# Kernel optimization log

Measured on AMD Instinct MI355X. Metric: run time of the kernel, lower is better.

The kernel has to match this reference:

```python
import jax, jax.numpy as jnp
import numpy as np

NUM_IT = 5            # init_kwargs num_it
N_NODES = 200_000
N_EDGES = 6_400_000   # avg degree 32
N_INIT_COLORS = 16

# odd 32-bit mixing constants (Knuth / xxhash primes); uint32 mults wrap mod 2^32
M1 = np.uint32(2654435761)
M2 = np.uint32(2246822519)
M3 = np.uint32(3266489917)
M4 = np.uint32(668265263)


def setup_inputs() -> dict:
    key = jax.random.key(0)
    k1, k2 = jax.random.split(key)
    x = jax.random.randint(k1, (N_NODES,), 0, N_INIT_COLORS, dtype=jnp.int32)
    edge_index = jax.random.randint(k2, (2, N_EDGES), 0, N_NODES, dtype=jnp.int32)
    return {"x": x, "edge_index": edge_index}


def _wl_iteration(colors, row, col, num_nodes):
    """One WLConv step: new color = id of (own color, sorted multiset of neighbor colors).

    The torch WLConv sorts each node's neighbor colors, hashes the tuple, and
    assigns compact ids via a dict. Here we do the same math vectorized:
    lexsort edges by (row, neighbor color), compute a position-weighted 2x32-bit
    hash of the sorted per-node sequence via segment_sum, mix in the node's own
    color, then relabel distinct keys to compact ids 0..k-1 with jnp.unique.
    """
    E = row.shape[0]
    c = colors[col]                                   # neighbor colors per edge [E]
    order = jnp.lexsort((c, row))                     # sort by node, then by color
    r_s = row[order]                                  # [E] sorted rows
    c_s = c[order].astype(jnp.uint32)                 # [E] sorted neighbor colors

    ones = jnp.ones((E,), dtype=jnp.int32)
    deg = jax.ops.segment_sum(ones, row, num_segments=num_nodes)      # [N]
    start = jnp.cumsum(deg) - deg                                     # segment offsets [N]
    pos = (jnp.arange(E, dtype=jnp.int32) - start[r_s]).astype(jnp.uint32)  # rank within node

    # two independent position-weighted hash lanes over each sorted neighbor list
    lane1 = jax.ops.segment_sum((c_s + 1) * (pos * M1 + M2), r_s, num_segments=num_nodes)
    lane2 = jax.ops.segment_sum((c_s + 1) * (pos * M3 + M4), r_s, num_segments=num_nodes)

    own = colors.astype(jnp.uint32) + 1
    key2 = jnp.stack([lane1 * M2 + own * M1, lane2 * M4 + own * M3], axis=1)  # [N,2]

    # dict-style relabeling: distinct keys -> compact ids (at most N distinct)
    _, inv = jnp.unique(key2, axis=0, size=num_nodes, return_inverse=True,
                        fill_value=jnp.uint32(0))
    return inv.reshape(-1).astype(colors.dtype)


def reference(x, edge_index):
    row, col = edge_index[0], edge_index[1]
    colors = x.astype(jnp.int32)
    for _ in range(NUM_IT):  # fixed small layer loop, not a data-dim loop
        colors = _wl_iteration(colors, row, col, N_NODES)
    return colors
```

## Files before the change

kernel.cpp:

```cpp
#include <hip/hip_runtime.h>
#include <stdint.h>

typedef unsigned int u32;
typedef unsigned long long u64;

#define M1 2654435761u
#define M2 2246822519u
#define M3 3266489917u
#define M4 668265263u
#define NUM_IT 5
#define PCHUNK 16384
#define HCH 65536
#define TILE 4096
#define PBCH 4096
#define CCAP 16384
#define SB 64
#define CHB 33
#define NKB 1024
#define KCH 4096
#define SCH 8192


__global__ void k_init(const int* __restrict__ x, int* __restrict__ colors,
                       u32* __restrict__ bcnt5, u32* __restrict__ bhist,
                       u32* __restrict__ cnt3, int n, int nbuck) {
    int i = blockIdx.x * blockDim.x + threadIdx.x;
    if (i < n) colors[i] = x[i];
    if (i < NUM_IT * NKB) bcnt5[i] = 0u;
    if (i >= 8192 && i < 8192 + nbuck) bhist[i - 8192] = 0u;
    if (i >= 16384 && i < 16384 + 48) cnt3[i - 16384] = 0u;
}

__global__ void k_chist(const int* __restrict__ row, u32* __restrict__ bhist,
                        u32* __restrict__ thist, int e, int nbuck) {
    __shared__ u32 fineh[1024];
    __shared__ u32 shist[16 * SB];
    int t = threadIdx.x;
    fineh[t] = 0u;
    shist[t] = 0u;
    __syncthreads();
    int c0 = blockIdx.x * HCH;
    int ce = c0 + HCH; if (ce > e) ce = e;
    int k = 0;
    for (int i = c0 + t; i < ce; i += 1024, ++k) {
        u32 r = (u32)row[i];
        atomicAdd(&fineh[r >> 8], 1u);
        atomicAdd(&shist[((k >> 2) << 6) | (r >> 12)], 1u);
    }
    __syncthreads();
    if (t < nbuck) {
        u32 v = fineh[t];
        if (v) atomicAdd(&bhist[t], v);
    }
    {
        int m = t >> 6;
        if (c0 + m * TILE < e)
            thist[(size_t)(blockIdx.x * 16 + m) * SB + (t & 63)] = shist[t];
    }
}

__global__ void k_cscan(const u32* __restrict__ bhist, u32* __restrict__ boffE,
                        u32* __restrict__ bcur, u32* __restrict__ boffS,
                        int nbuck, int nbS) {
    __shared__ u32 sh[256];
    u32 run = 0u;
    for (int base = 0; base < nbuck; base += 256) {
        int id = base + threadIdx.x;
        u32 x = (id < nbuck) ? bhist[id] : 0u;
        sh[threadIdx.x] = x;
        __syncthreads();
        for (int o = 1; o < 256; o <<= 1) {
            u32 t = (threadIdx.x >= (u32)o) ? sh[threadIdx.x - o] : 0u;
            __syncthreads();
            sh[threadIdx.x] += t;
            __syncthreads();
        }
        if (id < nbuck) {
            u32 excl = sh[threadIdx.x] - x + run;
            boffE[id] = excl;
            bcur[id] = excl;
            if ((id & 15) == 0) boffS[id >> 4] = excl;
        }
        u32 tot = sh[255];
        __syncthreads();
        run += tot;
    }
    if (threadIdx.x == 0) { boffE[nbuck] = run; boffS[nbS] = run; }
}

__global__ void k_tscan(const u32* __restrict__ thist, const u32* __restrict__ boffS,
                        u32* __restrict__ tbase, int ntiles) {
    __shared__ u32 sh[256];
    int b = blockIdx.x;
    int t = threadIdx.x;
    u32 run = boffS[b];
    for (int base = 0; base < ntiles; base += 256) {
        int tile = base + t;
        u32 x = (tile < ntiles) ? thist[(size_t)tile * SB + b] : 0u;
        sh[t] = x;
        __syncthreads();
        for (int o = 1; o < 256; o <<= 1) {
            u32 y = (t >= o) ? sh[t - o] : 0u;
            __syncthreads();
            sh[t] += y;
            __syncthreads();
        }
        if (tile < ntiles) tbase[(size_t)tile * SB + b] = run + sh[t] - x;
        u32 tot = sh[255];
        __syncthreads();
        run += tot;
    }
}

__global__ void k_partA(const int* __restrict__ row, const int* __restrict__ col,
                        const u32* __restrict__ thist, const u32* __restrict__ tbase,
                        u32* __restrict__ adjt, int e) {
    __shared__ u32 vals[TILE];
    __shared__ unsigned char bkt[TILE];
    __shared__ u32 lbase[SB + 1], gbase[SB], cur[SB];
    int t = threadIdx.x;
    int c0 = blockIdx.x * TILE;
    int ce = c0 + TILE; if (ce > e) ce = e;
    if (t < SB) {
        gbase[t] = tbase[(size_t)blockIdx.x * SB + t];
        cur[t] = 0u;
        lbase[t] = thist[(size_t)blockIdx.x * SB + t];
    }
    __syncthreads();
    if (t == 0) {
        u32 run = 0u;
        for (int b = 0; b < SB; ++b) { u32 h = lbase[b]; lbase[b] = run; run += h; }
        lbase[SB] = run;
    }
    __syncthreads();
    for (int i = c0 + t; i < ce; i += 256) {
        u32 r = (u32)row[i];
        u32 s = r >> 12;
        u32 p = lbase[s] + atomicAdd(&cur[s], 1u);
        vals[p] = ((r & 4095u) << 18) | (u32)col[i];
        bkt[p] = (unsigned char)s;
    }
    __syncthreads();
    int cnt = ce - c0;
    for (int i = t; i < cnt; i += 256) {
        u32 b = (u32)bkt[i];
        adjt[gbase[b] + ((u32)i - lbase[b])] = vals[i];
    }
}

__global__ void k_partB(const u32* __restrict__ adjt, const u32* __restrict__ boffS,
                        u32* __restrict__ ecur, u32* __restrict__ adj) {
    __shared__ u32 vals[PBCH];
    __shared__ u32 hist[16], lbase[17], gbase[16], cur[16];
    int s = blockIdx.x / CHB, c = blockIdx.x % CHB;
    u32 lo = boffS[s] + (u32)c * PBCH;
    u32 hi = boffS[s + 1];
    if (lo >= hi) return;
    if (hi > lo + PBCH) hi = lo + PBCH;
    int t = threadIdx.x;
    if (t < 16) hist[t] = 0u;
    __syncthreads();
    for (u32 i = lo + t; i < hi; i += 256)
        atomicAdd(&hist[(adjt[i] >> 26) & 15u], 1u);
    __syncthreads();
    if (t == 0) {
        u32 run = 0u;
        for (int b = 0; b < 16; ++b) { lbase[b] = run; run += hist[b]; }
        lbase[16] = run;
    }
    __syncthreads();
    if (t < 16) {
        u32 h = hist[t];
        gbase[t] = h ? atomicAdd(&ecur[s * 16 + t], h) : 0u;
        cur[t] = 0u;
    }
    __syncthreads();
    for (u32 i = lo + t; i < hi; i += 256) {
        u32 v = adjt[i];
        u32 b = (v >> 26) & 15u;
        vals[lbase[b] + atomicAdd(&cur[b], 1u)] = v;
    }
    __syncthreads();
    u32 cnt = hi - lo;
    for (u32 i = t; i < cnt; i += 256) {
        u32 v = vals[i];
        u32 b = (v >> 26) & 15u;
        adj[gbase[b] + (i - lbase[b])] = v & 0x03FFFFFFu;
    }
}

__global__ void k_part(const int* __restrict__ row, const int* __restrict__ col,
                       u32* __restrict__ bcur, u32* __restrict__ adjp, int e, int nbuck) {
    __shared__ u32 hist[1024], base[1024], cur[1024];
    int c0 = blockIdx.x * PCHUNK;
    int cend = c0 + PCHUNK; if (cend > e) cend = e;
    for (int t = threadIdx.x; t < nbuck; t += 256) hist[t] = 0u;
    __syncthreads();
    for (int i = c0 + threadIdx.x; i < cend; i += 256)
        atomicAdd(&hist[((u32)row[i]) >> 8], 1u);
    __syncthreads();
    for (int t = threadIdx.x; t < nbuck; t += 256) {
        u32 h = hist[t];
        base[t] = h ? atomicAdd(&bcur[t], h) : 0u;
        cur[t] = 0u;
    }
    __syncthreads();
    for (int i = c0 + threadIdx.x; i < cend; i += 256) {
        u32 r = (u32)row[i];
        u32 b = r >> 8;
        u32 local = atomicAdd(&cur[b], 1u);
        adjp[base[b] + local] = ((r & 255u) << 18) | (u32)col[i];
    }
}

__global__ void k_csr(u32* __restrict__ adj, const u32* __restrict__ boffE,
                      u32* __restrict__ deg, u32* __restrict__ start,
                      u32* __restrict__ lists, u32* __restrict__ cnt3, int n) {
    __shared__ u32 buf[CCAP];
    __shared__ u32 cnt[256], loc[256], cur[256];
    __shared__ u32 ch[3], cbase[3];
    int b = blockIdx.x;
    int v0 = b << 8;
    u32 bs = boffE[b], be = boffE[b + 1];
    int c = (int)(be - bs);
    if (c > CCAP) c = CCAP;
    cnt[threadIdx.x] = 0u;
    if (threadIdx.x < 3) ch[threadIdx.x] = 0u;
    for (int i = threadIdx.x; i < c; i += 256) buf[i] = adj[bs + i];
    __syncthreads();
    for (int i = threadIdx.x; i < c; i += 256)
        atomicAdd(&cnt[buf[i] >> 18], 1u);
    __syncthreads();
    u32 myc = cnt[threadIdx.x];
    loc[threadIdx.x] = myc;
    __syncthreads();
    for (int o = 1; o < 256; o <<= 1) {
        u32 t = (threadIdx.x >= (u32)o) ? loc[threadIdx.x - o] : 0u;
        __syncthreads();
        loc[threadIdx.x] += t;
        __syncthreads();
    }
    u32 excl = loc[threadIdx.x] - myc;
    int v = v0 + (int)threadIdx.x;
    u32 cls = 0u, crk = 0u;
    if (v < n) {
        deg[v] = myc; start[v] = bs + excl;
        cls = (myc <= 32u) ? 0u : ((myc <= 64u) ? 1u : 2u);
        crk = atomicAdd(&ch[cls], 1u);
    }
    cur[threadIdx.x] = bs + excl;
    __syncthreads();
    if (threadIdx.x < 3)
        cbase[threadIdx.x] = ch[threadIdx.x] ? atomicAdd(&cnt3[threadIdx.x * 16], ch[threadIdx.x]) : 0u;
    __syncthreads();
    if (v < n) lists[cls * (u32)n + cbase[cls] + crk] = (u32)v;
    for (int i = threadIdx.x; i < c; i += 256) {
        u32 p = buf[i];
        u32 q = atomicAdd(&cur[p >> 18], 1u);
        adj[q] = p & 0x3FFFFu;
    }
}


__device__ __forceinline__ void ce_reg(u32& a, u32& b, bool up) {
    u32 mn = a < b ? a : b, mx = a < b ? b : a;
    a = up ? mn : mx; b = up ? mx : mn;
}
__device__ __forceinline__ void ce_shf(u32& a, int o, bool tm) {
    u32 ot = (u32)__shfl_xor((int)a, o, 64);
    u32 mn = a < ot ? a : ot, mx = a < ot ? ot : a;
    a = tm ? mn : mx;
}
#define CE_SH4(o, tm) { ce_shf(c0, o, tm); ce_shf(c1, o, tm); ce_shf(c2, o, tm); ce_shf(c3, o, tm); }
#define CE_RG4(up)    { ce_reg(c0, c2, up); ce_reg(c1, c3, up); ce_reg(c0, c1, up); ce_reg(c2, c3, up); }

__global__ void k_hash(const int* __restrict__ colors, const u32* __restrict__ deg,
                       const u32* __restrict__ start, const u32* __restrict__ adj,
                       const u32* __restrict__ lists, const u32* __restrict__ cnt3,
                       u64* __restrict__ keys, int n) {
    int lane = threadIdx.x & 63;
    int wid = (int)((blockIdx.x * 256u + threadIdx.x) >> 6);
    u32 nA = cnt3[0], nBc = cnt3[16], nCc = cnt3[32];
    int octA = (int)((nA + 7u) >> 3);
    int quadB = (int)((nBc + 3u) >> 2);
    if (wid < octA) {
        int s = lane & 7;
        int li = 8 * wid + (lane >> 3);
        int node = (li < (int)nA) ? (int)lists[li] : -1;
        u32 c0 = 0xFFFFFFFFu, c1 = 0xFFFFFFFFu, c2 = 0xFFFFFFFFu, c3 = 0xFFFFFFFFu;
        u32 e0 = 4u * (u32)s;
        if (node >= 0) {
            u32 d = deg[node], st = start[node];
            if (e0 + 0u < d) c0 = (u32)colors[adj[st + e0 + 0u]];
            if (e0 + 1u < d) c1 = (u32)colors[adj[st + e0 + 1u]];
            if (e0 + 2u < d) c2 = (u32)colors[adj[st + e0 + 2u]];
            if (e0 + 3u < d) c3 = (u32)colors[adj[st + e0 + 3u]];
        }
        bool s1 = (s & 1) == 0, s2 = (s & 2) == 0, s4 = (s & 4) == 0;
        ce_reg(c0, c1, true); ce_reg(c2, c3, false);
        CE_RG4(s1)
        CE_SH4(1, s1 == s2)
        CE_RG4(s2)
        CE_SH4(2, s2 == s4)
        CE_SH4(1, s1 == s4)
        CE_RG4(s4)
        CE_SH4(4, s4)
        CE_SH4(2, s2)
        CE_SH4(1, s1)
        CE_RG4(true)
        u32 v = (c0 + 1u) * (e0 * M1 + M2) + (c1 + 1u) * ((e0 + 1u) * M1 + M2)
              + (c2 + 1u) * ((e0 + 2u) * M1 + M2) + (c3 + 1u) * ((e0 + 3u) * M1 + M2);
        u32 w = (c0 + 1u) * (e0 * M3 + M4) + (c1 + 1u) * ((e0 + 1u) * M3 + M4)
              + (c2 + 1u) * ((e0 + 2u) * M3 + M4) + (c3 + 1u) * ((e0 + 3u) * M3 + M4);
#pragma unroll
        for (int o = 1; o < 8; o <<= 1) {
            v += (u32)__shfl_xor((int)v, o, 64);
            w += (u32)__shfl_xor((int)w, o, 64);
        }
        if (s == 0 && node >= 0) {
            u32 own = (u32)colors[node] + 1u;
            keys[node] = ((u64)(v * M2 + own * M1) << 32) | (u64)(w * M4 + own * M3);
        }
    } else if (wid < octA + quadB) {
        int s = lane & 15;
        int li = 4 * (wid - octA) + (lane >> 4);
        int node = (li < (int)nBc) ? (int)lists[(u32)n + (u32)li] : -1;
        u32 c0 = 0xFFFFFFFFu, c1 = 0xFFFFFFFFu, c2 = 0xFFFFFFFFu, c3 = 0xFFFFFFFFu;
        u32 e0 = 4u * (u32)s;
        if (node >= 0) {
            u32 d = deg[node], st = start[node];
            if (e0 + 0u < d) c0 = (u32)colors[adj[st + e0 + 0u]];
            if (e0 + 1u < d) c1 = (u32)colors[adj[st + e0 + 1u]];
            if (e0 + 2u < d) c2 = (u32)colors[adj[st + e0 + 2u]];
            if (e0 + 3u < d) c3 = (u32)colors[adj[st + e0 + 3u]];
        }
        bool s1 = (s & 1) == 0, s2 = (s & 2) == 0, s4 = (s & 4) == 0, s8 = (s & 8) == 0;
        ce_reg(c0, c1, true); ce_reg(c2, c3, false);
        CE_RG4(s1)
        CE_SH4(1, s1 == s2)
        CE_RG4(s2)
        CE_SH4(2, s2 == s4)
        CE_SH4(1, s1 == s4)
        CE_RG4(s4)
        CE_SH4(4, s4 == s8)
        CE_SH4(2, s2 == s8)
        CE_SH4(1, s1 == s8)
        CE_RG4(s8)
        CE_SH4(8, s8)
        CE_SH4(4, s4)
        CE_SH4(2, s2)
        CE_SH4(1, s1)
        CE_RG4(true)
        u32 v = (c0 + 1u) * (e0 * M1 + M2) + (c1 + 1u) * ((e0 + 1u) * M1 + M2)
              + (c2 + 1u) * ((e0 + 2u) * M1 + M2) + (c3 + 1u) * ((e0 + 3u) * M1 + M2);
        u32 w = (c0 + 1u) * (e0 * M3 + M4) + (c1 + 1u) * ((e0 + 1u) * M3 + M4)
              + (c2 + 1u) * ((e0 + 2u) * M3 + M4) + (c3 + 1u) * ((e0 + 3u) * M3 + M4);
#pragma unroll
        for (int o = 1; o < 16; o <<= 1) {
            v += (u32)__shfl_xor((int)v, o, 64);
            w += (u32)__shfl_xor((int)w, o, 64);
        }
        if (s == 0 && node >= 0) {
            u32 own = (u32)colors[node] + 1u;
            keys[node] = ((u64)(v * M2 + own * M1) << 32) | (u64)(w * M4 + own * M3);
        }
    } else if (wid < octA + quadB + (int)nCc) {
        int node = (int)lists[2u * (u32)n + (u32)(wid - octA - quadB)];
        u32 d = deg[node], st = start[node];
        u32 v = 0u, w = 0u;
        for (u32 i = (u32)lane; i < d; i += 64u) {
            u32 ci = (u32)colors[adj[st + i]];
            u32 pos = 0u;
            for (u32 j = 0; j < d; ++j) {
                u32 cj = (u32)colors[adj[st + j]];
                pos += (cj < ci) || (cj == ci && j < i);
            }
            v += (ci + 1u) * (pos * M1 + M2);
            w += (ci + 1u) * (pos * M3 + M4);
        }
        for (int o = 32; o > 0; o >>= 1) {
            v += (u32)__shfl_xor((int)v, o, 64);
            w += (u32)__shfl_xor((int)w, o, 64);
        }
        if (lane == 0) {
            u32 own = (u32)colors[node] + 1u;
            keys[node] = ((u64)(v * M2 + own * M1) << 32) | (u64)(w * M4 + own * M3);
        }
    }
}


__global__ void k_khist(const u64* __restrict__ keys, u32* __restrict__ bcnt, int n) {
    __shared__ u32 h[NKB];
    int t = threadIdx.x;
    for (int i = t; i < NKB; i += 256) h[i] = 0u;
    __syncthreads();
    int c0 = blockIdx.x * KCH;
    int ce = c0 + KCH; if (ce > n) ce = n;
    for (int i = c0 + t; i < ce; i += 256)
        atomicAdd(&h[(u32)(keys[i] >> 54)], 1u);
    __syncthreads();
    for (int i = t; i < NKB; i += 256) {
        u32 v = h[i];
        if (v) atomicAdd(&bcnt[i], v);
    }
}

__global__ void k_bscan(const u32* __restrict__ cnt, u32* __restrict__ boff,
                        u32* __restrict__ bcurk) {
    int l = threadIdx.x;
    u32 v[16]; u32 s = 0u;
#pragma unroll
    for (int i = 0; i < 16; ++i) { v[i] = cnt[l * 16 + i]; s += v[i]; }
    u32 ps = s;
#pragma unroll
    for (int o = 1; o < 64; o <<= 1) {
        u32 t = (u32)__shfl_up((int)ps, o, 64);
        if (l >= o) ps += t;
    }
    u32 run = ps - s;
#pragma unroll
    for (int i = 0; i < 16; ++i) {
        boff[l * 16 + i] = run;
        bcurk[l * 16 + i] = run;
        run += v[i];
    }
    if (l == 63) boff[NKB] = run;
}

__global__ void k_scatter(const u64* __restrict__ keys, u64* __restrict__ out,
                          u32* __restrict__ nout, u32* __restrict__ cur, int n) {
    __shared__ u32 h[NKB], base[NKB];
    int t = threadIdx.x;
    h[t] = 0u;
    __syncthreads();
    int c0 = blockIdx.x * SCH;
    u64 k[8]; u32 r[8];
#pragma unroll
    for (int i = 0; i < 8; ++i) {
        int id = c0 + t + i * 1024;
        if (id < n) { k[i] = keys[id]; r[i] = atomicAdd(&h[(u32)(k[i] >> 54)], 1u); }
    }
    __syncthreads();
    base[t] = h[t] ? atomicAdd(&cur[t], h[t]) : 0u;
    __syncthreads();
#pragma unroll
    for (int i = 0; i < 8; ++i) {
        int id = c0 + t + i * 1024;
        if (id < n) {
            u32 p = base[(u32)(k[i] >> 54)] + r[i];
            out[p] = k[i];
            nout[p] = (u32)id;
        }
    }
}

__global__ void k_bsort(u64* __restrict__ data, u32* __restrict__ nidx,
                        const u32* __restrict__ boff,
                        u32* __restrict__ comb, u32* __restrict__ dcount) {
    __shared__ u64 sh[512];
    __shared__ u32 pid[512];
    __shared__ u32 ts[256];
    int b = blockIdx.x;
    u32 lo = boff[b];
    int cnt = (int)(boff[b + 1] - lo);
    if (cnt > 512) cnt = 512;
    int m = (cnt <= 256) ? 256 : 512;
    int t = threadIdx.x;
    for (int i = t; i < m; i += 256) {
        sh[i] = (i < cnt) ? data[lo + i] : ~0ULL;
        pid[i] = (i < cnt) ? nidx[lo + i] : 0u;
    }
    __syncthreads();
    for (int k = 2; k <= m; k <<= 1) {
        for (int j = k >> 1; j > 0; j >>= 1) {
            for (int e = t; e < m; e += 256) {
                int p = e ^ j;
                if (p > e) {
                    u64 a = sh[e], c = sh[p];
                    bool up = ((e & k) == 0);
                    if (up ? (a > c) : (a < c)) {
                        sh[e] = c; sh[p] = a;
                        u32 tp = pid[e]; pid[e] = pid[p]; pid[p] = tp;
                    }
                }
            }
            __syncthreads();
        }
    }
    int i0 = 2 * t, i1 = 2 * t + 1;
    u32 f0 = (i0 < cnt) ? ((i0 == 0) ? 1u : (sh[i0] != sh[i0 - 1] ? 1u : 0u)) : 0u;
    u32 f1 = (i1 < cnt) ? (sh[i1] != sh[i1 - 1] ? 1u : 0u) : 0u;
    u32 s2 = f0 + f1;
    ts[t] = s2;
    __syncthreads();
    for (int o = 1; o < 256; o <<= 1) {
        u32 x = (t >= o) ? ts[t - o] : 0u;
        __syncthreads();
        ts[t] += x;
        __syncthreads();
    }
    u32 excl = ts[t] - s2;
    u32 tag = (u32)b << 16;
    if (i0 < cnt) { nidx[lo + i0] = pid[i0]; comb[lo + i0] = tag | (excl + f0); }
    if (i1 < cnt) { nidx[lo + i1] = pid[i1]; comb[lo + i1] = tag | (excl + f0 + f1); }
    if (t == 255) dcount[b] = ts[255];
}

__global__ void k_dscan(const u32* __restrict__ dcount, u32* __restrict__ dbase) {
    int l = threadIdx.x;
    u32 v[16]; u32 s = 0u;
#pragma unroll
    for (int i = 0; i < 16; ++i) { v[i] = dcount[l * 16 + i]; s += v[i]; }
    u32 ps = s;
#pragma unroll
    for (int o = 1; o < 64; o <<= 1) {
        u32 t = (u32)__shfl_up((int)ps, o, 64);
        if (l >= o) ps += t;
    }
    u32 run = ps - s;
#pragma unroll
    for (int i = 0; i < 16; ++i) {
        dbase[l * 16 + i] = run;
        run += v[i];
    }
}

__global__ void k_relabel(const u32* __restrict__ comb, const u32* __restrict__ nidx,
                          const u32* __restrict__ dbase, int* __restrict__ colors, int n) {
    int i = blockIdx.x * blockDim.x + threadIdx.x;
    if (i >= n) return;
    u32 c = comb[i];
    colors[nidx[i]] = (int)(dbase[c >> 16] + (c & 0xFFFFu) - 1u);
}


extern "C" void kernel_launch(void* const* d_in, const int* in_sizes, int n_in,
                              void* d_out, int out_size, void* d_ws, size_t ws_size,
                              hipStream_t stream) {
    const int* x = (const int*)d_in[0];
    const int* ei = (const int*)d_in[1];
    const int N = in_sizes[0];
    const int E = in_sizes[1] / 2;
    const int* row = ei;
    const int* col = ei + E;
    int* colors = (int*)d_out;

    const int ntiles = (E + TILE - 1) / TILE;

    char* ws = (char*)d_ws;
    size_t off = 0;
#define WS_ALLOC(T, name, bytes) T name = (T)(ws + off); off += (((size_t)(bytes)) + 255) & ~(size_t)255;
    WS_ALLOC(u32*, deg, (size_t)N * 4)
    WS_ALLOC(u32*, start, (size_t)N * 4)
    WS_ALLOC(u32*, adj, (size_t)E * 4)
    WS_ALLOC(u64*, keys, (size_t)N * 8)
    WS_ALLOC(u64*, sorted, (size_t)N * 8)
    WS_ALLOC(u32*, nidx, (size_t)N * 4)
    WS_ALLOC(u32*, comb, (size_t)N * 4)
    WS_ALLOC(u32*, bcnt5, (size_t)NUM_IT * NKB * 4)
    WS_ALLOC(u32*, boff, (NKB + 1) * 4)
    WS_ALLOC(u32*, bcurk, NKB * 4)
    WS_ALLOC(u32*, dcount, NKB * 4)
    WS_ALLOC(u32*, dbase, NKB * 4)
    WS_ALLOC(u32*, bhist, 1024 * 4)
    WS_ALLOC(u32*, boffE, 1025 * 4)
    WS_ALLOC(u32*, bcur, 1024 * 4)
    WS_ALLOC(u32*, boffS, (SB + 1) * 4)
    WS_ALLOC(u32*, cnt3, 48 * 4)
    WS_ALLOC(u32*, thist, (size_t)ntiles * SB * 4)
    WS_ALLOC(u32*, tbase, (size_t)ntiles * SB * 4)
    u32* adjt = (u32*)(ws + off);
    u32* lists = adjt;
    const bool two_level = (off + (size_t)E * 4 <= ws_size) && ((size_t)3 * N <= (size_t)E);
#undef WS_ALLOC

    const int nB = (N + 255) / 256;
    const int nbuck = (N + 255) >> 8;
    const int nbS = (nbuck + 15) >> 4;
    const int kB = (N + KCH - 1) / KCH;
    const int sBk = (N + SCH - 1) / SCH;

    k_init<<<nB, 256, 0, stream>>>(x, colors, bcnt5, bhist, cnt3, N, nbuck);
    k_chist<<<(E + HCH - 1) / HCH, 1024, 0, stream>>>(row, bhist, thist, E, nbuck);
    k_cscan<<<1, 256, 0, stream>>>(bhist, boffE, bcur, boffS, nbuck, nbS);
    if (two_level) {
        k_tscan<<<nbS, 256, 0, stream>>>(thist, boffS, tbase, ntiles);
        k_partA<<<ntiles, 256, 0, stream>>>(row, col, thist, tbase, adjt, E);
        k_partB<<<nbS * CHB, 256, 0, stream>>>(adjt, boffS, bcur, adj);
    } else {
        k_part<<<(E + PCHUNK - 1) / PCHUNK, 256, 0, stream>>>(row, col, bcur, adj, E, nbuck);
    }
    k_csr<<<nbuck, 256, 0, stream>>>(adj, boffE, deg, start, lists, cnt3, N);

    for (int it = 0; it < NUM_IT; ++it) {
        u32* bcnt = bcnt5 + it * NKB;
        k_hash<<<(N + 3) / 4, 256, 0, stream>>>(colors, deg, start, adj, lists, cnt3, keys, N);
        k_khist<<<kB, 256, 0, stream>>>(keys, bcnt, N);
        k_bscan<<<1, 64, 0, stream>>>(bcnt, boff, bcurk);
        k_scatter<<<sBk, 1024, 0, stream>>>(keys, sorted, nidx, bcurk, N);
        k_bsort<<<NKB, 256, 0, stream>>>(sorted, nidx, boff, comb, dcount);
        k_dscan<<<1, 64, 0, stream>>>(dcount, dbase);
        k_relabel<<<nB, 256, 0, stream>>>(comb, nidx, dbase, colors, N);
    }
}
```

Measured before the change: 661.2 us.

## Fuse bucket scans into scatter/relabel and widen per-lane sort to 8 elements

Removes the two single-block scan kernels per iteration by recomputing the 1024-bucket prefix sums redundantly inside each k_scatter and k_relabel block. The scatter now uses a per-iteration zeroed cursor array plus the local offsets. Separately, k_hash gives each lane 8 neighbour colours instead of 4, so the bitonic sort needs fewer cross-lane shuffles and more nodes fit per wave. The cost is redundant scan work in every block and higher register pressure in k_hash.

```diff
diff --git a/kernel.cpp b/kernel.cpp
--- a/kernel.cpp
+++ b/kernel.cpp
@@ -26,8 +26,8 @@
                        u32* __restrict__ cnt3, int n, int nbuck) {
     int i = blockIdx.x * blockDim.x + threadIdx.x;
     if (i < n) colors[i] = x[i];
-    if (i < NUM_IT * NKB) bcnt5[i] = 0u;
-    if (i >= 8192 && i < 8192 + nbuck) bhist[i - 8192] = 0u;
+    if (i < 2 * NUM_IT * NKB) bcnt5[i] = 0u;
+    if (i >= 12288 && i < 12288 + nbuck) bhist[i - 12288] = 0u;
     if (i >= 16384 && i < 16384 + 48) cnt3[i - 16384] = 0u;
 }
 
@@ -271,8 +271,33 @@
     u32 mn = a < ot ? a : ot, mx = a < ot ? ot : a;
     a = tm ? mn : mx;
 }
-#define CE_SH4(o, tm) { ce_shf(c0, o, tm); ce_shf(c1, o, tm); ce_shf(c2, o, tm); ce_shf(c3, o, tm); }
-#define CE_RG4(up)    { ce_reg(c0, c2, up); ce_reg(c1, c3, up); ce_reg(c0, c1, up); ce_reg(c2, c3, up); }
+#define SH8(o, tm) { ce_shf(c0,o,tm); ce_shf(c1,o,tm); ce_shf(c2,o,tm); ce_shf(c3,o,tm); \
+                     ce_shf(c4,o,tm); ce_shf(c5,o,tm); ce_shf(c6,o,tm); ce_shf(c7,o,tm); }
+#define RG8(up) { ce_reg(c0,c4,up); ce_reg(c1,c5,up); ce_reg(c2,c6,up); ce_reg(c3,c7,up); \
+                  ce_reg(c0,c2,up); ce_reg(c1,c3,up); ce_reg(c4,c6,up); ce_reg(c5,c7,up); \
+                  ce_reg(c0,c1,up); ce_reg(c2,c3,up); ce_reg(c4,c5,up); ce_reg(c6,c7,up); }
+#define K2R { ce_reg(c0,c1,true); ce_reg(c2,c3,false); ce_reg(c4,c5,true); ce_reg(c6,c7,false); }
+#define K4R { ce_reg(c0,c2,true); ce_reg(c1,c3,true); ce_reg(c4,c6,false); ce_reg(c5,c7,false); \
+              ce_reg(c0,c1,true); ce_reg(c2,c3,true); ce_reg(c4,c5,false); ce_reg(c6,c7,false); }
+#define LOAD8(dd, stt) { \
+    if (e0 + 0u < (dd)) c0 = (u32)colors[adj[(stt) + e0 + 0u]]; \
+    if (e0 + 1u < (dd)) c1 = (u32)colors[adj[(stt) + e0 + 1u]]; \
+    if (e0 + 2u < (dd)) c2 = (u32)colors[adj[(stt) + e0 + 2u]]; \
+    if (e0 + 3u < (dd)) c3 = (u32)colors[adj[(stt) + e0 + 3u]]; \
+    if (e0 + 4u < (dd)) c4 = (u32)colors[adj[(stt) + e0 + 4u]]; \
+    if (e0 + 5u < (dd)) c5 = (u32)colors[adj[(stt) + e0 + 5u]]; \
+    if (e0 + 6u < (dd)) c6 = (u32)colors[adj[(stt) + e0 + 6u]]; \
+    if (e0 + 7u < (dd)) c7 = (u32)colors[adj[(stt) + e0 + 7u]]; }
+#define HASHVW \
+    u32 a1 = e0 * M1, a3 = e0 * M3; \
+    u32 v = (c0 + 1u) * (a1 + M2)            + (c1 + 1u) * (a1 + 1u*M1 + M2) \
+          + (c2 + 1u) * (a1 + 2u*M1 + M2)    + (c3 + 1u) * (a1 + 3u*M1 + M2) \
+          + (c4 + 1u) * (a1 + 4u*M1 + M2)    + (c5 + 1u) * (a1 + 5u*M1 + M2) \
+          + (c6 + 1u) * (a1 + 6u*M1 + M2)    + (c7 + 1u) * (a1 + 7u*M1 + M2); \
+    u32 w = (c0 + 1u) * (a3 + M4)            + (c1 + 1u) * (a3 + 1u*M3 + M4) \
+          + (c2 + 1u) * (a3 + 2u*M3 + M4)    + (c3 + 1u) * (a3 + 3u*M3 + M4) \
+          + (c4 + 1u) * (a3 + 4u*M3 + M4)    + (c5 + 1u) * (a3 + 5u*M3 + M4) \
+          + (c6 + 1u) * (a3 + 6u*M3 + M4)    + (c7 + 1u) * (a3 + 7u*M3 + M4);
 
 __global__ void k_hash(const int* __restrict__ colors, const u32* __restrict__ deg,
                        const u32* __restrict__ start, const u32* __restrict__ adj,
@@ -281,91 +306,59 @@
     int lane = threadIdx.x & 63;
     int wid = (int)((blockIdx.x * 256u + threadIdx.x) >> 6);
     u32 nA = cnt3[0], nBc = cnt3[16], nCc = cnt3[32];
-    int octA = (int)((nA + 7u) >> 3);
-    int quadB = (int)((nBc + 3u) >> 2);
-    if (wid < octA) {
-        int s = lane & 7;
-        int li = 8 * wid + (lane >> 3);
+    int hexA = (int)((nA + 15u) >> 4);
+    int octB = (int)((nBc + 7u) >> 3);
+    if (wid < hexA) {
+        int s = lane & 3;
+        int li = 16 * wid + (lane >> 2);
         int node = (li < (int)nA) ? (int)lists[li] : -1;
-        u32 c0 = 0xFFFFFFFFu, c1 = 0xFFFFFFFFu, c2 = 0xFFFFFFFFu, c3 = 0xFFFFFFFFu;
-        u32 e0 = 4u * (u32)s;
+        u32 c0 = ~0u, c1 = ~0u, c2 = ~0u, c3 = ~0u, c4 = ~0u, c5 = ~0u, c6 = ~0u, c7 = ~0u;
+        u32 e0 = 8u * (u32)s;
         if (node >= 0) {
             u32 d = deg[node], st = start[node];
-            if (e0 + 0u < d) c0 = (u32)colors[adj[st + e0 + 0u]];
-            if (e0 + 1u < d) c1 = (u32)colors[adj[st + e0 + 1u]];
-            if (e0 + 2u < d) c2 = (u32)colors[adj[st + e0 + 2u]];
-            if (e0 + 3u < d) c3 = (u32)colors[adj[st + e0 + 3u]];
-        }
-        bool s1 = (s & 1) == 0, s2 = (s & 2) == 0, s4 = (s & 4) == 0;
-        ce_reg(c0, c1, true); ce_reg(c2, c3, false);
-        CE_RG4(s1)
-        CE_SH4(1, s1 == s2)
-        CE_RG4(s2)
-        CE_SH4(2, s2 == s4)
-        CE_SH4(1, s1 == s4)
-        CE_RG4(s4)
-        CE_SH4(4, s4)
-        CE_SH4(2, s2)
-        CE_SH4(1, s1)
-        CE_RG4(true)
-        u32 v = (c0 + 1u) * (e0 * M1 + M2) + (c1 + 1u) * ((e0 + 1u) * M1 + M2)
-              + (c2 + 1u) * ((e0 + 2u) * M1 + M2) + (c3 + 1u) * ((e0 + 3u) * M1 + M2);
-        u32 w = (c0 + 1u) * (e0 * M3 + M4) + (c1 + 1u) * ((e0 + 1u) * M3 + M4)
-              + (c2 + 1u) * ((e0 + 2u) * M3 + M4) + (c3 + 1u) * ((e0 + 3u) * M3 + M4);
-#pragma unroll
-        for (int o = 1; o < 8; o <<= 1) {
-            v += (u32)__shfl_xor((int)v, o, 64);
-            w += (u32)__shfl_xor((int)w, o, 64);
-        }
+            LOAD8(d, st)
+        }
+        bool s1 = (s & 1) == 0, s2 = (s & 2) == 0;
+        K2R
+        K4R
+        RG8(s1)
+        SH8(1, s1 == s2) RG8(s2)
+        SH8(2, s2) SH8(1, s1) RG8(true)
+        HASHVW
+        v += (u32)__shfl_xor((int)v, 1, 64); v += (u32)__shfl_xor((int)v, 2, 64);
+        w += (u32)__shfl_xor((int)w, 1, 64); w += (u32)__shfl_xor((int)w, 2, 64);
         if (s == 0 && node >= 0) {
             u32 own = (u32)colors[node] + 1u;
             keys[node] = ((u64)(v * M2 + own * M1) << 32) | (u64)(w * M4 + own * M3);
         }
-    } else if (wid < octA + quadB) {
-        int s = lane & 15;
-        int li = 4 * (wid - octA) + (lane >> 4);
+    } else if (wid < hexA + octB) {
+        int s = lane & 7;
+        int li = 8 * (wid - hexA) + (lane >> 3);
         int node = (li < (int)nBc) ? (int)lists[(u32)n + (u32)li] : -1;
-        u32 c0 = 0xFFFFFFFFu, c1 = 0xFFFFFFFFu, c2 = 0xFFFFFFFFu, c3 = 0xFFFFFFFFu;
-        u32 e0 = 4u * (u32)s;
+        u32 c0 = ~0u, c1 = ~0u, c2 = ~0u, c3 = ~0u, c4 = ~0u, c5 = ~0u, c6 = ~0u, c7 = ~0u;
+        u32 e0 = 8u * (u32)s;
         if (node >= 0) {
             u32 d = deg[node], st = start[node];
-            if (e0 + 0u < d) c0 = (u32)colors[adj[st + e0 + 0u]];
-            if (e0 + 1u < d) c1 = (u32)colors[adj[st + e0 + 1u]];
-            if (e0 + 2u < d) c2 = (u32)colors[adj[st + e0 + 2u]];
-            if (e0 + 3u < d) c3 = (u32)colors[adj[st + e0 + 3u]];
-        }
-        bool s1 = (s & 1) == 0, s2 = (s & 2) == 0, s4 = (s & 4) == 0, s8 = (s & 8) == 0;
-        ce_reg(c0, c1, true); ce_reg(c2, c3, false);
-        CE_RG4(s1)
-        CE_SH4(1, s1 == s2)
-        CE_RG4(s2)
-        CE_SH4(2, s2 == s4)
-        CE_SH4(1, s1 == s4)
-        CE_RG4(s4)
-        CE_SH4(4, s4 == s8)
-        CE_SH4(2, s2 == s8)
-        CE_SH4(1, s1 == s8)
-        CE_RG4(s8)
-        CE_SH4(8, s8)
-        CE_SH4(4, s4)
-        CE_SH4(2, s2)
-        CE_SH4(1, s1)
-        CE_RG4(true)
-        u32 v = (c0 + 1u) * (e0 * M1 + M2) + (c1 + 1u) * ((e0 + 1u) * M1 + M2)
-              + (c2 + 1u) * ((e0 + 2u) * M1 + M2) + (c3 + 1u) * ((e0 + 3u) * M1 + M2);
-        u32 w = (c0 + 1u) * (e0 * M3 + M4) + (c1 + 1u) * ((e0 + 1u) * M3 + M4)
-              + (c2 + 1u) * ((e0 + 2u) * M3 + M4) + (c3 + 1u) * ((e0 + 3u) * M3 + M4);
-#pragma unroll
-        for (int o = 1; o < 16; o <<= 1) {
-            v += (u32)__shfl_xor((int)v, o, 64);
-            w += (u32)__shfl_xor((int)w, o, 64);
-        }
+            LOAD8(d, st)
+        }
+        bool s1 = (s & 1) == 0, s2 = (s & 2) == 0, s4 = (s & 4) == 0;
+        K2R
+        K4R
+        RG8(s1)
+        SH8(1, s1 == s2) RG8(s2)
+        SH8(2, s2 == s4) SH8(1, s1 == s4) RG8(s4)
+        SH8(4, s4) SH8(2, s2) SH8(1, s1) RG8(true)
+        HASHVW
+        v += (u32)__shfl_xor((int)v, 1, 64); v += (u32)__shfl_xor((int)v, 2, 64);
+        v += (u32)__shfl_xor((int)v, 4, 64);
+        w += (u32)__shfl_xor((int)w, 1, 64); w += (u32)__shfl_xor((int)w, 2, 64);
+        w += (u32)__shfl_xor((int)w, 4, 64);
         if (s == 0 && node >= 0) {
             u32 own = (u32)colors[node] + 1u;
             keys[node] = ((u64)(v * M2 + own * M1) << 32) | (u64)(w * M4 + own * M3);
         }
-    } else if (wid < octA + quadB + (int)nCc) {
-        int node = (int)lists[2u * (u32)n + (u32)(wid - octA - quadB)];
+    } else if (wid < hexA + octB + (int)nCc) {
+        int node = (int)lists[2u * (u32)n + (u32)(wid - hexA - octB)];
         u32 d = deg[node], st = start[node];
         u32 v = 0u, w = 0u;
         for (u32 i = (u32)lane; i < d; i += 64u) {
@@ -406,34 +399,31 @@
     }
 }
 
-__global__ void k_bscan(const u32* __restrict__ cnt, u32* __restrict__ boff,
-                        u32* __restrict__ bcurk) {
-    int l = threadIdx.x;
-    u32 v[16]; u32 s = 0u;
-#pragma unroll
-    for (int i = 0; i < 16; ++i) { v[i] = cnt[l * 16 + i]; s += v[i]; }
-    u32 ps = s;
-#pragma unroll
-    for (int o = 1; o < 64; o <<= 1) {
-        u32 t = (u32)__shfl_up((int)ps, o, 64);
-        if (l >= o) ps += t;
-    }
-    u32 run = ps - s;
-#pragma unroll
-    for (int i = 0; i < 16; ++i) {
-        boff[l * 16 + i] = run;
-        bcurk[l * 16 + i] = run;
-        run += v[i];
-    }
-    if (l == 63) boff[NKB] = run;
-}
-
 __global__ void k_scatter(const u64* __restrict__ keys, u64* __restrict__ out,
-                          u32* __restrict__ nout, u32* __restrict__ cur, int n) {
-    __shared__ u32 h[NKB], base[NKB];
+                          u32* __restrict__ nout, const u32* __restrict__ bcnt,
+                          u32* __restrict__ cur, u32* __restrict__ boff, int n) {
+    __shared__ u32 h[NKB], base[NKB], boffL[NKB];
     int t = threadIdx.x;
     h[t] = 0u;
-    __syncthreads();
+    if (t < 64) {
+        u32 v[16]; u32 s = 0u;
+#pragma unroll
+        for (int i = 0; i < 16; ++i) { v[i] = bcnt[t * 16 + i]; s += v[i]; }
+        u32 ps = s;
+#pragma unroll
+        for (int o = 1; o < 64; o <<= 1) {
+            u32 y = (u32)__shfl_up((int)ps, o, 64);
+            if (t >= o) ps += y;
+        }
+        u32 run = ps - s;
+#pragma unroll
+        for (int i = 0; i < 16; ++i) { boffL[t * 16 + i] = run; run += v[i]; }
+    }
+    __syncthreads();
+    if (blockIdx.x == 0) {
+        boff[t] = boffL[t];
+        if (t == 0) boff[NKB] = boffL[NKB - 1] + bcnt[NKB - 1];
+    }
     int c0 = blockIdx.x * SCH;
     u64 k[8]; u32 r[8];
 #pragma unroll
@@ -442,7 +432,7 @@
         if (id < n) { k[i] = keys[id]; r[i] = atomicAdd(&h[(u32)(k[i] >> 54)], 1u); }
     }
     __syncthreads();
-    base[t] = h[t] ? atomicAdd(&cur[t], h[t]) : 0u;
+    base[t] = boffL[t] + (h[t] ? atomicAdd(&cur[t], h[t]) : 0u);
     __syncthreads();
 #pragma unroll
     for (int i = 0; i < 8; ++i) {
@@ -507,31 +497,29 @@
     if (t == 255) dcount[b] = ts[255];
 }
 
-__global__ void k_dscan(const u32* __restrict__ dcount, u32* __restrict__ dbase) {
-    int l = threadIdx.x;
-    u32 v[16]; u32 s = 0u;
-#pragma unroll
-    for (int i = 0; i < 16; ++i) { v[i] = dcount[l * 16 + i]; s += v[i]; }
-    u32 ps = s;
-#pragma unroll
-    for (int o = 1; o < 64; o <<= 1) {
-        u32 t = (u32)__shfl_up((int)ps, o, 64);
-        if (l >= o) ps += t;
-    }
-    u32 run = ps - s;
-#pragma unroll
-    for (int i = 0; i < 16; ++i) {
-        dbase[l * 16 + i] = run;
-        run += v[i];
-    }
-}
-
 __global__ void k_relabel(const u32* __restrict__ comb, const u32* __restrict__ nidx,
-                          const u32* __restrict__ dbase, int* __restrict__ colors, int n) {
-    int i = blockIdx.x * blockDim.x + threadIdx.x;
+                          const u32* __restrict__ dcount, int* __restrict__ colors, int n) {
+    __shared__ u32 dbaseL[NKB];
+    int t = threadIdx.x;
+    if (t < 64) {
+        u32 v[16]; u32 s = 0u;
+#pragma unroll
+        for (int i = 0; i < 16; ++i) { v[i] = dcount[t * 16 + i]; s += v[i]; }
+        u32 ps = s;
+#pragma unroll
+        for (int o = 1; o < 64; o <<= 1) {
+            u32 y = (u32)__shfl_up((int)ps, o, 64);
+            if (t >= o) ps += y;
+        }
+        u32 run = ps - s;
+#pragma unroll
+        for (int i = 0; i < 16; ++i) { dbaseL[t * 16 + i] = run; run += v[i]; }
+    }
+    __syncthreads();
+    int i = blockIdx.x * 256 + t;
     if (i >= n) return;
     u32 c = comb[i];
-    colors[nidx[i]] = (int)(dbase[c >> 16] + (c & 0xFFFFu) - 1u);
+    colors[nidx[i]] = (int)(dbaseL[c >> 16] + (c & 0xFFFFu) - 1u);
 }
 
 
@@ -558,11 +546,9 @@
     WS_ALLOC(u64*, sorted, (size_t)N * 8)
     WS_ALLOC(u32*, nidx, (size_t)N * 4)
     WS_ALLOC(u32*, comb, (size_t)N * 4)
-    WS_ALLOC(u32*, bcnt5, (size_t)NUM_IT * NKB * 4)
+    WS_ALLOC(u32*, bcnt5, (size_t)2 * NUM_IT * NKB * 4)
     WS_ALLOC(u32*, boff, (NKB + 1) * 4)
-    WS_ALLOC(u32*, bcurk, NKB * 4)
     WS_ALLOC(u32*, dcount, NKB * 4)
-    WS_ALLOC(u32*, dbase, NKB * 4)
     WS_ALLOC(u32*, bhist, 1024 * 4)
     WS_ALLOC(u32*, boffE, 1025 * 4)
     WS_ALLOC(u32*, bcur, 1024 * 4)
@@ -595,12 +581,11 @@
 
     for (int it = 0; it < NUM_IT; ++it) {
         u32* bcnt = bcnt5 + it * NKB;
+        u32* bcur_it = bcnt5 + (NUM_IT + it) * NKB;
         k_hash<<<(N + 3) / 4, 256, 0, stream>>>(colors, deg, start, adj, lists, cnt3, keys, N);
         k_khist<<<kB, 256, 0, stream>>>(keys, bcnt, N);
-        k_bscan<<<1, 64, 0, stream>>>(bcnt, boff, bcurk);
-        k_scatter<<<sBk, 1024, 0, stream>>>(keys, sorted, nidx, bcurk, N);
+        k_scatter<<<sBk, 1024, 0, stream>>>(keys, sorted, nidx, bcnt, bcur_it, boff, N);
         k_bsort<<<NKB, 256, 0, stream>>>(sorted, nidx, boff, comb, dcount);
-        k_dscan<<<1, 64, 0, stream>>>(dcount, dbase);
-        k_relabel<<<nB, 256, 0, stream>>>(comb, nidx, dbase, colors, N);
-    }
-}
+        k_relabel<<<nB, 256, 0, stream>>>(comb, nidx, dcount, colors, N);
+    }
+}
```

Result: no change. 669.3 us (+1.2%).

## Fold scan kernels into scatter/relabel and pack node metadata into list entries

Applied to the files above, without the earlier changes.

Removes the two single-block scan kernels per iteration (bucket-offset scan and distinct-count scan). Each scatter and relabel block now recomputes the 1024-entry prefix sum redundantly in shared memory, with per-iteration zeroed cursor arrays. Node lists are widened to 64-bit entries packing start, clamped degree and node id, so the hash kernel skips separate deg/start loads for small and medium nodes. This saves launches and serialized tiny kernels. The cost is redundant scan work in every block, and the two-level partition path now needs a larger edge-to-node ratio.

```diff
diff --git a/kernel.cpp b/kernel.cpp
--- a/kernel.cpp
+++ b/kernel.cpp
@@ -26,8 +26,8 @@
                        u32* __restrict__ cnt3, int n, int nbuck) {
     int i = blockIdx.x * blockDim.x + threadIdx.x;
     if (i < n) colors[i] = x[i];
-    if (i < NUM_IT * NKB) bcnt5[i] = 0u;
-    if (i >= 8192 && i < 8192 + nbuck) bhist[i - 8192] = 0u;
+    if (i < 2 * NUM_IT * NKB) bcnt5[i] = 0u;
+    if (i >= 12288 && i < 12288 + nbuck) bhist[i - 12288] = 0u;
     if (i >= 16384 && i < 16384 + 48) cnt3[i - 16384] = 0u;
 }
 
@@ -215,7 +215,7 @@
 
 __global__ void k_csr(u32* __restrict__ adj, const u32* __restrict__ boffE,
                       u32* __restrict__ deg, u32* __restrict__ start,
-                      u32* __restrict__ lists, u32* __restrict__ cnt3, int n) {
+                      u64* __restrict__ lists, u32* __restrict__ cnt3, int n) {
     __shared__ u32 buf[CCAP];
     __shared__ u32 cnt[256], loc[256], cur[256];
     __shared__ u32 ch[3], cbase[3];
@@ -253,7 +253,11 @@
     if (threadIdx.x < 3)
         cbase[threadIdx.x] = ch[threadIdx.x] ? atomicAdd(&cnt3[threadIdx.x * 16], ch[threadIdx.x]) : 0u;
     __syncthreads();
-    if (v < n) lists[cls * (u32)n + cbase[cls] + crk] = (u32)v;
+    if (v < n) {
+        u32 dcl = myc > 0x3FFFu ? 0x3FFFu : myc;
+        lists[cls * (size_t)n + cbase[cls] + crk] =
+            ((u64)((dcl << 18) | (u32)v) << 32) | (u64)(bs + excl);
+    }
     for (int i = threadIdx.x; i < c; i += 256) {
         u32 p = buf[i];
         u32 q = atomicAdd(&cur[p >> 18], 1u);
@@ -276,7 +280,7 @@
 
 __global__ void k_hash(const int* __restrict__ colors, const u32* __restrict__ deg,
                        const u32* __restrict__ start, const u32* __restrict__ adj,
-                       const u32* __restrict__ lists, const u32* __restrict__ cnt3,
+                       const u64* __restrict__ lists, const u32* __restrict__ cnt3,
                        u64* __restrict__ keys, int n) {
     int lane = threadIdx.x & 63;
     int wid = (int)((blockIdx.x * 256u + threadIdx.x) >> 6);
@@ -286,11 +290,15 @@
     if (wid < octA) {
         int s = lane & 7;
         int li = 8 * wid + (lane >> 3);
-        int node = (li < (int)nA) ? (int)lists[li] : -1;
+        int node = -1;
         u32 c0 = 0xFFFFFFFFu, c1 = 0xFFFFFFFFu, c2 = 0xFFFFFFFFu, c3 = 0xFFFFFFFFu;
         u32 e0 = 4u * (u32)s;
-        if (node >= 0) {
-            u32 d = deg[node], st = start[node];
+        if (li < (int)nA) {
+            u64 pk = lists[li];
+            u32 st = (u32)pk;
+            u32 hi = (u32)(pk >> 32);
+            u32 d = hi >> 18;
+            node = (int)(hi & 0x3FFFFu);
             if (e0 + 0u < d) c0 = (u32)colors[adj[st + e0 + 0u]];
             if (e0 + 1u < d) c1 = (u32)colors[adj[st + e0 + 1u]];
             if (e0 + 2u < d) c2 = (u32)colors[adj[st + e0 + 2u]];
@@ -308,10 +316,11 @@
         CE_SH4(2, s2)
         CE_SH4(1, s1)
         CE_RG4(true)
-        u32 v = (c0 + 1u) * (e0 * M1 + M2) + (c1 + 1u) * ((e0 + 1u) * M1 + M2)
-              + (c2 + 1u) * ((e0 + 2u) * M1 + M2) + (c3 + 1u) * ((e0 + 3u) * M1 + M2);
-        u32 w = (c0 + 1u) * (e0 * M3 + M4) + (c1 + 1u) * ((e0 + 1u) * M3 + M4)
-              + (c2 + 1u) * ((e0 + 2u) * M3 + M4) + (c3 + 1u) * ((e0 + 3u) * M3 + M4);
+        u32 a1 = e0 * M1, a3 = e0 * M3;
+        u32 v = (c0 + 1u) * (a1 + M2)           + (c1 + 1u) * (a1 + 1u * M1 + M2)
+              + (c2 + 1u) * (a1 + 2u * M1 + M2) + (c3 + 1u) * (a1 + 3u * M1 + M2);
+        u32 w = (c0 + 1u) * (a3 + M4)           + (c1 + 1u) * (a3 + 1u * M3 + M4)
+              + (c2 + 1u) * (a3 + 2u * M3 + M4) + (c3 + 1u) * (a3 + 3u * M3 + M4);
 #pragma unroll
         for (int o = 1; o < 8; o <<= 1) {
             v += (u32)__shfl_xor((int)v, o, 64);
@@ -324,11 +333,15 @@
     } else if (wid < octA + quadB) {
         int s = lane & 15;
         int li = 4 * (wid - octA) + (lane >> 4);
-        int node = (li < (int)nBc) ? (int)lists[(u32)n + (u32)li] : -1;
+        int node = -1;
         u32 c0 = 0xFFFFFFFFu, c1 = 0xFFFFFFFFu, c2 = 0xFFFFFFFFu, c3 = 0xFFFFFFFFu;
         u32 e0 = 4u * (u32)s;
-        if (node >= 0) {
-            u32 d = deg[node], st = start[node];
+        if (li < (int)nBc) {
+            u64 pk = lists[(size_t)n + (u32)li];
+            u32 st = (u32)pk;
+            u32 hi = (u32)(pk >> 32);
+            u32 d = hi >> 18;
+            node = (int)(hi & 0x3FFFFu);
             if (e0 + 0u < d) c0 = (u32)colors[adj[st + e0 + 0u]];
             if (e0 + 1u < d) c1 = (u32)colors[adj[st + e0 + 1u]];
             if (e0 + 2u < d) c2 = (u32)colors[adj[st + e0 + 2u]];
@@ -351,10 +364,11 @@
         CE_SH4(2, s2)
         CE_SH4(1, s1)
         CE_RG4(true)
-        u32 v = (c0 + 1u) * (e0 * M1 + M2) + (c1 + 1u) * ((e0 + 1u) * M1 + M2)
-              + (c2 + 1u) * ((e0 + 2u) * M1 + M2) + (c3 + 1u) * ((e0 + 3u) * M1 + M2);
-        u32 w = (c0 + 1u) * (e0 * M3 + M4) + (c1 + 1u) * ((e0 + 1u) * M3 + M4)
-              + (c2 + 1u) * ((e0 + 2u) * M3 + M4) + (c3 + 1u) * ((e0 + 3u) * M3 + M4);
+        u32 a1 = e0 * M1, a3 = e0 * M3;
+        u32 v = (c0 + 1u) * (a1 + M2)           + (c1 + 1u) * (a1 + 1u * M1 + M2)
+              + (c2 + 1u) * (a1 + 2u * M1 + M2) + (c3 + 1u) * (a1 + 3u * M1 + M2);
+        u32 w = (c0 + 1u) * (a3 + M4)           + (c1 + 1u) * (a3 + 1u * M3 + M4)
+              + (c2 + 1u) * (a3 + 2u * M3 + M4) + (c3 + 1u) * (a3 + 3u * M3 + M4);
 #pragma unroll
         for (int o = 1; o < 16; o <<= 1) {
             v += (u32)__shfl_xor((int)v, o, 64);
@@ -365,8 +379,10 @@
             keys[node] = ((u64)(v * M2 + own * M1) << 32) | (u64)(w * M4 + own * M3);
         }
     } else if (wid < octA + quadB + (int)nCc) {
-        int node = (int)lists[2u * (u32)n + (u32)(wid - octA - quadB)];
-        u32 d = deg[node], st = start[node];
+        u64 pk = lists[2u * (size_t)n + (u32)(wid - octA - quadB)];
+        int node = (int)((u32)(pk >> 32) & 0x3FFFFu);
+        u32 st = (u32)pk;
+        u32 d = deg[node];
         u32 v = 0u, w = 0u;
         for (u32 i = (u32)lane; i < d; i += 64u) {
             u32 ci = (u32)colors[adj[st + i]];
@@ -406,34 +422,31 @@
     }
 }
 
-__global__ void k_bscan(const u32* __restrict__ cnt, u32* __restrict__ boff,
-                        u32* __restrict__ bcurk) {
-    int l = threadIdx.x;
-    u32 v[16]; u32 s = 0u;
-#pragma unroll
-    for (int i = 0; i < 16; ++i) { v[i] = cnt[l * 16 + i]; s += v[i]; }
-    u32 ps = s;
-#pragma unroll
-    for (int o = 1; o < 64; o <<= 1) {
-        u32 t = (u32)__shfl_up((int)ps, o, 64);
-        if (l >= o) ps += t;
-    }
-    u32 run = ps - s;
-#pragma unroll
-    for (int i = 0; i < 16; ++i) {
-        boff[l * 16 + i] = run;
-        bcurk[l * 16 + i] = run;
-        run += v[i];
-    }
-    if (l == 63) boff[NKB] = run;
-}
-
 __global__ void k_scatter(const u64* __restrict__ keys, u64* __restrict__ out,
-                          u32* __restrict__ nout, u32* __restrict__ cur, int n) {
-    __shared__ u32 h[NKB], base[NKB];
+                          u32* __restrict__ nout, const u32* __restrict__ bcnt,
+                          u32* __restrict__ cur, u32* __restrict__ boff, int n) {
+    __shared__ u32 h[NKB], base[NKB], boffL[NKB];
     int t = threadIdx.x;
     h[t] = 0u;
-    __syncthreads();
+    if (t < 64) {
+        u32 v[16]; u32 s = 0u;
+#pragma unroll
+        for (int i = 0; i < 16; ++i) { v[i] = bcnt[t * 16 + i]; s += v[i]; }
+        u32 ps = s;
+#pragma unroll
+        for (int o = 1; o < 64; o <<= 1) {
+            u32 y = (u32)__shfl_up((int)ps, o, 64);
+            if (t >= o) ps += y;
+        }
+        u32 run = ps - s;
+#pragma unroll
+        for (int i = 0; i < 16; ++i) { boffL[t * 16 + i] = run; run += v[i]; }
+    }
+    __syncthreads();
+    if (blockIdx.x == 0) {
+        boff[t] = boffL[t];
+        if (t == 0) boff[NKB] = boffL[NKB - 1] + bcnt[NKB - 1];
+    }
     int c0 = blockIdx.x * SCH;
     u64 k[8]; u32 r[8];
 #pragma unroll
@@ -442,7 +455,7 @@
         if (id < n) { k[i] = keys[id]; r[i] = atomicAdd(&h[(u32)(k[i] >> 54)], 1u); }
     }
     __syncthreads();
-    base[t] = h[t] ? atomicAdd(&cur[t], h[t]) : 0u;
+    base[t] = boffL[t] + (h[t] ? atomicAdd(&cur[t], h[t]) : 0u);
     __syncthreads();
 #pragma unroll
     for (int i = 0; i < 8; ++i) {
@@ -507,31 +520,29 @@
     if (t == 255) dcount[b] = ts[255];
 }
 
-__global__ void k_dscan(const u32* __restrict__ dcount, u32* __restrict__ dbase) {
-    int l = threadIdx.x;
-    u32 v[16]; u32 s = 0u;
-#pragma unroll
-    for (int i = 0; i < 16; ++i) { v[i] = dcount[l * 16 + i]; s += v[i]; }
-    u32 ps = s;
-#pragma unroll
-    for (int o = 1; o < 64; o <<= 1) {
-        u32 t = (u32)__shfl_up((int)ps, o, 64);
-        if (l >= o) ps += t;
-    }
-    u32 run = ps - s;
-#pragma unroll
-    for (int i = 0; i < 16; ++i) {
-        dbase[l * 16 + i] = run;
-        run += v[i];
-    }
-}
-
 __global__ void k_relabel(const u32* __restrict__ comb, const u32* __restrict__ nidx,
-                          const u32* __restrict__ dbase, int* __restrict__ colors, int n) {
-    int i = blockIdx.x * blockDim.x + threadIdx.x;
+                          const u32* __restrict__ dcount, int* __restrict__ colors, int n) {
+    __shared__ u32 dbaseL[NKB];
+    int t = threadIdx.x;
+    if (t < 64) {
+        u32 v[16]; u32 s = 0u;
+#pragma unroll
+        for (int i = 0; i < 16; ++i) { v[i] = dcount[t * 16 + i]; s += v[i]; }
+        u32 ps = s;
+#pragma unroll
+        for (int o = 1; o < 64; o <<= 1) {
+            u32 y = (u32)__shfl_up((int)ps, o, 64);
+            if (t >= o) ps += y;
+        }
+        u32 run = ps - s;
+#pragma unroll
+        for (int i = 0; i < 16; ++i) { dbaseL[t * 16 + i] = run; run += v[i]; }
+    }
+    __syncthreads();
+    int i = blockIdx.x * 256 + t;
     if (i >= n) return;
     u32 c = comb[i];
-    colors[nidx[i]] = (int)(dbase[c >> 16] + (c & 0xFFFFu) - 1u);
+    colors[nidx[i]] = (int)(dbaseL[c >> 16] + (c & 0xFFFFu) - 1u);
 }
 
 
@@ -558,11 +569,9 @@
     WS_ALLOC(u64*, sorted, (size_t)N * 8)
     WS_ALLOC(u32*, nidx, (size_t)N * 4)
     WS_ALLOC(u32*, comb, (size_t)N * 4)
-    WS_ALLOC(u32*, bcnt5, (size_t)NUM_IT * NKB * 4)
+    WS_ALLOC(u32*, bcnt5, (size_t)2 * NUM_IT * NKB * 4)
     WS_ALLOC(u32*, boff, (NKB + 1) * 4)
-    WS_ALLOC(u32*, bcurk, NKB * 4)
     WS_ALLOC(u32*, dcount, NKB * 4)
-    WS_ALLOC(u32*, dbase, NKB * 4)
     WS_ALLOC(u32*, bhist, 1024 * 4)
     WS_ALLOC(u32*, boffE, 1025 * 4)
     WS_ALLOC(u32*, bcur, 1024 * 4)
@@ -571,8 +580,8 @@
     WS_ALLOC(u32*, thist, (size_t)ntiles * SB * 4)
     WS_ALLOC(u32*, tbase, (size_t)ntiles * SB * 4)
     u32* adjt = (u32*)(ws + off);
-    u32* lists = adjt;
-    const bool two_level = (off + (size_t)E * 4 <= ws_size) && ((size_t)3 * N <= (size_t)E);
+    u64* lists = (u64*)(ws + off);
+    const bool two_level = (off + (size_t)E * 4 <= ws_size) && ((size_t)6 * N <= (size_t)E);
 #undef WS_ALLOC
 
     const int nB = (N + 255) / 256;
@@ -595,12 +604,11 @@
 
     for (int it = 0; it < NUM_IT; ++it) {
         u32* bcnt = bcnt5 + it * NKB;
+        u32* bcur_it = bcnt5 + (NUM_IT + it) * NKB;
         k_hash<<<(N + 3) / 4, 256, 0, stream>>>(colors, deg, start, adj, lists, cnt3, keys, N);
         k_khist<<<kB, 256, 0, stream>>>(keys, bcnt, N);
-        k_bscan<<<1, 64, 0, stream>>>(bcnt, boff, bcurk);
-        k_scatter<<<sBk, 1024, 0, stream>>>(keys, sorted, nidx, bcurk, N);
+        k_scatter<<<sBk, 1024, 0, stream>>>(keys, sorted, nidx, bcnt, bcur_it, boff, N);
         k_bsort<<<NKB, 256, 0, stream>>>(sorted, nidx, boff, comb, dcount);
-        k_dscan<<<1, 64, 0, stream>>>(dcount, dbase);
-        k_relabel<<<nB, 256, 0, stream>>>(comb, nidx, dbase, colors, N);
-    }
-}
+        k_relabel<<<nB, 256, 0, stream>>>(comb, nidx, dcount, colors, N);
+    }
+}
```

Measured after the change: 642.5 us. 1.03x faster.
